# Kernel tuning notes

Hardware: AMD Instinct MI355X
Metric: run time of the kernel (lower is better)

Reference implementation:

```python
import jax, jax.numpy as jnp
import numpy as np

EPS = 1e-5
CIN = [3, 24, 48, 96, 192]
COUT = [24, 48, 96, 192, 384]
P = 512
NUM_CLASSES = 101
FC_IN = 384 * 16 * 3 * 3  # 55296


def _poly_layer(x, proj, alpha, gamma, beta):
    # x: (B, C, D, H, W)
    B, C, D, H, W = x.shape
    # im2col: 3x3x3 patches with zero padding 1 -> (B, C*27, D, H, W)
    patches = jax.lax.conv_general_dilated_patches(
        x, filter_shape=(3, 3, 3), window_strides=(1, 1, 1),
        padding=[(1, 1), (1, 1), (1, 1)])
    patches = jnp.moveaxis(patches, 1, -1)  # (B, D, H, W, C*27)
    ws = jnp.einsum('bdhwk,pk->bdhwp', patches, proj)      # projector GEMM
    out = jnp.einsum('bdhwp,po->bdhwo', ws, alpha)         # alpha GEMM
    out = jnp.maximum(1.0 + out, 0.0)                      # clamp(1+x, min=0)
    out = jnp.moveaxis(out, -1, 1)                         # (B, O, D, H, W)
    # MaxPool3d kernel/stride (1,2,2)
    out = jax.lax.reduce_window(out, -jnp.inf, jax.lax.max,
                                (1, 1, 1, 2, 2), (1, 1, 1, 2, 2), 'VALID')
    # BatchNorm3d with batch statistics (train-mode math)
    mean = out.mean(axis=(0, 2, 3, 4), keepdims=True)
    var = out.var(axis=(0, 2, 3, 4), keepdims=True)
    out = (out - mean) * jax.lax.rsqrt(var + EPS)
    out = out * gamma.reshape(1, -1, 1, 1, 1) + beta.reshape(1, -1, 1, 1, 1)
    return out


def setup_inputs() -> dict:
    key = jax.random.key(0)
    keys = jax.random.split(key, 32)
    inp = {'x': jax.random.normal(keys[0], (2, 3, 16, 112, 112), dtype=jnp.float32)}
    ki = 1
    for i in range(5):
        k_feat = CIN[i] * 27
        inp[f'p{i+1}'] = jax.random.normal(keys[ki], (P, k_feat), dtype=jnp.float32) / np.sqrt(k_feat); ki += 1
        inp[f'a{i+1}'] = jax.random.normal(keys[ki], (P, COUT[i]), dtype=jnp.float32) * np.sqrt(2.0 / COUT[i]); ki += 1
        inp[f'g{i+1}'] = jnp.ones((COUT[i],), dtype=jnp.float32)
        inp[f'q{i+1}'] = jnp.zeros((COUT[i],), dtype=jnp.float32)
    inp['w1'] = jax.random.normal(keys[ki], (512, FC_IN), dtype=jnp.float32) * np.sqrt(2.0 / 512); ki += 1
    inp['b1'] = jnp.zeros((512,), dtype=jnp.float32)
    inp['w2'] = jax.random.normal(keys[ki], (256, 512), dtype=jnp.float32) * np.sqrt(2.0 / 256); ki += 1
    inp['b2'] = jnp.zeros((256,), dtype=jnp.float32)
    inp['w3'] = jax.random.normal(keys[ki], (NUM_CLASSES, 256), dtype=jnp.float32) * np.sqrt(2.0 / NUM_CLASSES); ki += 1
    inp['b3'] = jnp.zeros((NUM_CLASSES,), dtype=jnp.float32)
    return inp


def reference(x, p1, a1, g1, q1, p2, a2, g2, q2, p3, a3, g3, q3,
              p4, a4, g4, q4, p5, a5, g5, q5, w1, b1, w2, b2, w3, b3):
    projs = [p1, p2, p3, p4, p5]
    alphas = [a1, a2, a3, a4, a5]
    gammas = [g1, g2, g3, g4, g5]
    betas = [q1, q2, q3, q4, q5]
    h = x
    for i in range(5):
        h = _poly_layer(h, projs[i], alphas[i], gammas[i], betas[i])
    h = h.reshape(h.shape[0], -1)  # (B, 55296)
    h = jax.nn.relu(h @ w1.T + b1)  # dropout = identity (eval)
    h = jax.nn.relu(h @ w2.T + b2)
    logits = h @ w3.T + b3
    return logits
```

## Files before the change

kernel.cpp:

```cpp
#include <hip/hip_runtime.h>

#define EPS_BN 1e-5f

typedef __attribute__((ext_vector_type(8))) short sh8;
typedef __attribute__((ext_vector_type(4))) short sh4;
typedef __attribute__((ext_vector_type(4))) float f32x4;

static const size_t PART_OFF = 2645784;
static const size_t PRE_OFF  = 6258456;
static const size_t OUT5_OFF = 8666904;
static const size_t H_OFF    = 8777496;
static const size_t ST_OFF   = 8888088;
static const size_t BNP_OFF  = 8888856;
static const size_t H1_OFF   = 8938008;
static const size_t WS_TOT   = 8939032;
__device__ __align__(256) float g_ws[WS_TOT];

static const size_t XIN_OFF = 0;
static const size_t A1_OFF  = 1871424;
static const size_t A2_OFF  = 4776768;
static const size_t A3_OFF  = 6331968;
static const size_t A4_OFF  = 7216704;
static const size_t AR_TOT  = 7776576;
__device__ __align__(256) unsigned short g_act[AR_TOT];

static const size_t WB_OFF[5] = {0, 4096, 36352, 162304, 659968};
static const size_t WB_TOT    = 2650624;
__device__ __align__(256) unsigned short g_wb[WB_TOT];

__device__ inline unsigned short f2bf(float v) {
    unsigned u = __float_as_uint(v);
    return (unsigned short)((u + 0x7fffu + ((u >> 16) & 1u)) >> 16);
}
__device__ inline float bf2f(unsigned short h) {
    return __uint_as_float(((unsigned)h) << 16);
}

__global__ __launch_bounds__(256) void init_input(const float* __restrict__ x,
                                                  unsigned short* __restrict__ xp,
                                                  float* __restrict__ bnp,
                                                  int4* __restrict__ zp, int nz,
                                                  int4* __restrict__ wbz, int nwb)
{
    const int i = blockIdx.x * 256 + threadIdx.x;
    if (i < nz) zp[i] = make_int4(0, 0, 0, 0);
    if (i < nwb) wbz[i] = make_int4(0, 0, 0, 0);
    if (i < 49152) bnp[i] = 0.f;
    if (i >= 2 * 18 * 114 * 114 * 4) return;
    const int c = i & 3;
    int t = i >> 2;
    const int xx = t % 114; t /= 114;
    const int yy = t % 114; t /= 114;
    const int zz = t % 18;
    const int b  = t / 18;
    float v = 0.f;
    if (c < 3 && (unsigned)(zz - 1) < 16u && (unsigned)(yy - 1) < 112u && (unsigned)(xx - 1) < 112u)
        v = x[(((size_t)b * 3 + c) * 16 + (zz - 1)) * 12544 + (yy - 1) * 112 + (xx - 1)];
    xp[i] = f2bf(v);
}

struct PrepArgs {
    const float* src[10];
    int W[10];
    int dstrow[10];
    int start[11];
    int rowtot;
};

__global__ __launch_bounds__(256) void prep_t(PrepArgs a, unsigned short* __restrict__ dst)
{
    __shared__ unsigned short tileh[32 * 72];
    __shared__ unsigned short tilel[32 * 72];
    int m = 0;
    {
        const int bx = blockIdx.x;
        while (m < 9 && bx >= a.start[m + 1]) ++m;
    }
    const int t  = blockIdx.x - a.start[m];
    const int tw = t >> 4, tp = t & 15;
    const int p0 = tp * 32, w0 = tw * 64;
    const int W = a.W[m];
    const float* __restrict__ src = a.src[m];
    const int tid = threadIdx.x;

    #pragma unroll
    for (int e = 0; e < 8; ++e) {
        const int idx = tid + e * 256;
        const int w = idx & 63, pr = idx >> 6;
        const int gw = w0 + w;
        float v = 0.f;
        if (gw < W) v = src[(size_t)(p0 + pr) * W + gw];
        const unsigned short hh = f2bf(v);
        tileh[pr * 72 + w] = hh;
        tilel[pr * 72 + w] = f2bf(v - bf2f(hh));
    }
    __syncthreads();
    {
        const int wr = tid >> 2, pg = (tid & 3) * 8;
        sh8 packh, packl;
        #pragma unroll
        for (int e = 0; e < 8; ++e) {
            packh[e] = (short)tileh[(pg + e) * 72 + wr];
            packl[e] = (short)tilel[(pg + e) * 72 + wr];
        }
        const size_t rh = (size_t)a.dstrow[m] + w0 + wr;
        *(sh8*)&dst[rh * 512 + p0 + pg] = packh;
        *(sh8*)&dst[(rh + a.rowtot) * 512 + p0 + pg] = packl;
    }
}

struct Fuse3Args {
    int aoff[5], poff[5];
    int woff[5];
    int KL[5];
    int noft[5];
    int kt[5];
    int start[6];
    int rowtot;
};

__global__ __launch_bounds__(256) void fuse_mfma(const unsigned short* __restrict__ tb,
                                                 unsigned short* __restrict__ wlin,
                                                 Fuse3Args a)
{
    int l = 0;
    {
        const int bx = blockIdx.x;
        while (l < 4 && bx >= a.start[l + 1]) ++l;
    }
    const int idx = blockIdx.x - a.start[l];
    const int ot = idx / a.kt[l];
    const int kt = idx % a.kt[l];
    const int lane = threadIdx.x & 63;
    const int wv = threadIdx.x >> 6;
    const size_t LOFF = (size_t)a.rowtot * 512;
    const int f = ot * 4 + wv;
    if (f >= a.noft[l]) return;

    const unsigned short* arow = tb + ((size_t)(a.aoff[l] + f * 16 + (lane & 15))) * 512 + (lane >> 4) * 8;
    const unsigned short* brow = tb + ((size_t)(a.poff[l] + kt * 64 + (lane & 15))) * 512 + (lane >> 4) * 8;

    f32x4 acc[4];
    #pragma unroll
    for (int i = 0; i < 4; ++i) acc[i] = (f32x4){0.f, 0.f, 0.f, 0.f};

    #pragma unroll 2
    for (int p0 = 0; p0 < 512; p0 += 32) {
        const sh8 ah  = *(const sh8*)(arow + p0);
        const sh8 alo = *(const sh8*)(arow + LOFF + p0);
        #pragma unroll
        for (int nt = 0; nt < 4; ++nt) {
            const sh8 bh = *(const sh8*)(brow + (size_t)nt * 16 * 512 + p0);
            const sh8 bl = *(const sh8*)(brow + LOFF + (size_t)nt * 16 * 512 + p0);
            acc[nt] = __builtin_amdgcn_mfma_f32_16x16x32_bf16(ah, bh, acc[nt], 0, 0, 0);
            acc[nt] = __builtin_amdgcn_mfma_f32_16x16x32_bf16(ah, bl, acc[nt], 0, 0, 0);
            acc[nt] = __builtin_amdgcn_mfma_f32_16x16x32_bf16(alo, bh, acc[nt], 0, 0, 0);
        }
    }

    const int KL = a.KL[l];
    unsigned short* wrow = wlin + a.woff[l];
    #pragma unroll
    for (int nt = 0; nt < 4; ++nt) {
        const int k = kt * 64 + nt * 16 + (lane & 15);
        #pragma unroll
        for (int j = 0; j < 4; ++j) {
            const int o = f * 16 + (lane >> 4) * 4 + j;
            wrow[(size_t)o * KL + k] = f2bf(acc[nt][j]);
        }
    }
}

struct ReordBArgs {
    int woff[5], wboff[5];
    int K[5], KL[5], KP[5], CP[5];
    int start[6];
};

__global__ __launch_bounds__(256) void reorder_b(const unsigned short* __restrict__ wlin,
                                                 unsigned short* __restrict__ wb,
                                                 ReordBArgs a)
{
    __shared__ __align__(16) unsigned short lds[5184];
    int l = 0;
    {
        const int bx = blockIdx.x;
        while (l < 4 && bx >= a.start[l + 1]) ++l;
    }
    const int o = blockIdx.x - a.start[l];
    const int K = a.K[l], KL = a.KL[l], KP = a.KP[l], CP = a.CP[l];
    const int tid = threadIdx.x;
    for (int i = tid; i < KP; i += 256) lds[i] = 0;
    __syncthreads();
    const unsigned short* src = wlin + a.woff[l] + (size_t)o * KL;
    for (int k = tid; k < K; k += 256) {
        const int c = k / 27, s = k - c * 27;
        lds[s * CP + c] = src[k];
    }
    __syncthreads();
    unsigned short* drow = wb + a.wboff[l] + (size_t)o * KP;
    for (int i = tid * 8; i < KP; i += 2048)
        *(sh8*)&drow[i] = *(const sh8*)&lds[i];
}

template<int CPAD, int COUT, int KPAD, int HI, int WI, int HP, int WP, int NBLK, int SPLIT>
__global__ __launch_bounds__(256) void conv_mfma(
    const unsigned short* __restrict__ in, const unsigned short* __restrict__ Wb,
    float* __restrict__ outf, float* __restrict__ part, float* __restrict__ bnp)
{
    constexpr int NT = NBLK / 16;
    constexpr int HI2 = HI + 2, WI2 = WI + 2;
    constexpr bool C8 = (CPAD % 8 == 0);
    constexpr int TABN = C8 ? KPAD / 8 : KPAD / 4;
    constexpr int NSTEP = KPAD / 32 / SPLIT;
    constexpr int MTOT = 2 * 16 * HP * WP * 4;
    constexpr bool BONCE = (NBLK * KPAD * 2 <= 16384);
    constexpr int BROW = BONCE ? (KPAD + 8) : 40;
    constexpr int BS_ELEMS = BONCE ? NBLK * BROW : 2 * NBLK * 40;

    __shared__ __align__(16) unsigned short As[2][128 * 40];
    __shared__ __align__(16) unsigned short Bs[BS_ELEMS];
    __shared__ int tab[TABN];
    __shared__ float bs[(SPLIT == 1) ? 2 * NBLK : 1];

    const int tid = threadIdx.x;
    const int lane = tid & 63;
    const int wv = tid >> 6;
    const int blk_m = blockIdx.x;
    const int oc0 = blockIdx.y * NBLK;
    const int kc = (SPLIT > 1) ? blockIdx.z : 0;

    for (int i = tid; i < TABN; i += 256) {
        const int k = i * (C8 ? 8 : 4);
        const int s = k / CPAD, c = k % CPAD;
        tab[i] = (s < 27) ? ((((s / 9) * HI2 + (s % 9) / 3) * WI2 + (s % 3)) * CPAD + c) : -1;
    }

    if constexpr (BONCE) {
        for (int i = tid; i < NBLK * KPAD / 8; i += 256) {
            const int r = i / (KPAD / 8), kk = i - r * (KPAD / 8);
            *(sh8*)&Bs[r * BROW + kk * 8] = *(const sh8*)&Wb[(size_t)(oc0 + r) * KPAD + kk * 8];
        }
    }

    const int srow = tid >> 1;
    const int half = tid & 1;
    const int m_g = blk_m * 128 + srow;
    const int pooled_s = m_g >> 2, sub_s = m_g & 3;
    const int pw_g = pooled_s % WP;
    const int ph_g = (pooled_s / WP) % HP;
    const int d_g  = (pooled_s / (WP * HP)) & 15;
    const int b_g  = pooled_s / (WP * HP * 16);
    const int h_g = 2 * ph_g + (sub_s >> 1);
    const int w_g = 2 * pw_g + (sub_s & 1);
    const size_t base_m = ((((size_t)b_g * 18 + d_g) * HI2 + h_g) * WI2 + w_g) * CPAD;

    const int brow = tid >> 2, bcc = tid & 3;
    const bool bload = (tid < NBLK * 4);

    f32x4 acc[2][NT];
    #pragma unroll
    for (int mf = 0; mf < 2; ++mf)
        #pragma unroll
        for (int i = 0; i < NT; ++i) acc[mf][i] = (f32x4){0.f, 0.f, 0.f, 0.f};

    const int k_begin = kc * NSTEP * 32;

    sh8 aA0, aA1;
    sh4 aP0, aP1, aP2, aP3;
    sh8 brg;

    __syncthreads();

    {
        const int k0 = k_begin;
        if constexpr (C8) {
            const int o0 = tab[(k0 >> 3) + half * 2];
            const int o1 = tab[(k0 >> 3) + half * 2 + 1];
            aA0 = (sh8){0, 0, 0, 0, 0, 0, 0, 0};
            aA1 = (sh8){0, 0, 0, 0, 0, 0, 0, 0};
            if (o0 >= 0) aA0 = *(const sh8*)(in + base_m + o0);
            if (o1 >= 0) aA1 = *(const sh8*)(in + base_m + o1);
            *(sh8*)&As[0][srow * 40 + (half * 2) * 8]     = aA0;
            *(sh8*)&As[0][srow * 40 + (half * 2 + 1) * 8] = aA1;
        } else {
            const int t0 = tab[(k0 >> 2) + half * 4];
            const int t1 = tab[(k0 >> 2) + half * 4 + 1];
            const int t2 = tab[(k0 >> 2) + half * 4 + 2];
            const int t3 = tab[(k0 >> 2) + half * 4 + 3];
            aP0 = (sh4){0, 0, 0, 0}; aP1 = (sh4){0, 0, 0, 0};
            aP2 = (sh4){0, 0, 0, 0}; aP3 = (sh4){0, 0, 0, 0};
            if (t0 >= 0) aP0 = *(const sh4*)(in + base_m + t0);
            if (t1 >= 0) aP1 = *(const sh4*)(in + base_m + t1);
            if (t2 >= 0) aP2 = *(const sh4*)(in + base_m + t2);
            if (t3 >= 0) aP3 = *(const sh4*)(in + base_m + t3);
            *(sh4*)&As[0][srow * 40 + (half * 4) * 4]     = aP0;
            *(sh4*)&As[0][srow * 40 + (half * 4 + 1) * 4] = aP1;
            *(sh4*)&As[0][srow * 40 + (half * 4 + 2) * 4] = aP2;
            *(sh4*)&As[0][srow * 40 + (half * 4 + 3) * 4] = aP3;
        }
        if constexpr (!BONCE) {
            if (bload) {
                brg = *(const sh8*)&Wb[(size_t)(oc0 + brow) * KPAD + k0 + bcc * 8];
                *(sh8*)&Bs[0 + brow * 40 + bcc * 8] = brg;
            }
        }
    }
    __syncthreads();

    int cur = 0;
    for (int s = 0; s < NSTEP; ++s) {
        const int k0 = k_begin + s * 32;
        if (s + 1 < NSTEP) {
            const int kn = k0 + 32;
            if constexpr (C8) {
                const int o0 = tab[(kn >> 3) + half * 2];
                const int o1 = tab[(kn >> 3) + half * 2 + 1];
                aA0 = (sh8){0, 0, 0, 0, 0, 0, 0, 0};
                aA1 = (sh8){0, 0, 0, 0, 0, 0, 0, 0};
                if (o0 >= 0) aA0 = *(const sh8*)(in + base_m + o0);
                if (o1 >= 0) aA1 = *(const sh8*)(in + base_m + o1);
            } else {
                const int t0 = tab[(kn >> 2) + half * 4];
                const int t1 = tab[(kn >> 2) + half * 4 + 1];
                const int t2 = tab[(kn >> 2) + half * 4 + 2];
                const int t3 = tab[(kn >> 2) + half * 4 + 3];
                aP0 = (sh4){0, 0, 0, 0}; aP1 = (sh4){0, 0, 0, 0};
                aP2 = (sh4){0, 0, 0, 0}; aP3 = (sh4){0, 0, 0, 0};
                if (t0 >= 0) aP0 = *(const sh4*)(in + base_m + t0);
                if (t1 >= 0) aP1 = *(const sh4*)(in + base_m + t1);
                if (t2 >= 0) aP2 = *(const sh4*)(in + base_m + t2);
                if (t3 >= 0) aP3 = *(const sh4*)(in + base_m + t3);
            }
            if constexpr (!BONCE) {
                if (bload) brg = *(const sh8*)&Wb[(size_t)(oc0 + brow) * KPAD + kn + bcc * 8];
            }
        }
        const sh8 af0 = *(const sh8*)&As[cur][(wv * 16 + (lane & 15)) * 40 + (lane >> 4) * 8];
        const sh8 af1 = *(const sh8*)&As[cur][(64 + wv * 16 + (lane & 15)) * 40 + (lane >> 4) * 8];
        #pragma unroll
        for (int nt = 0; nt < NT; ++nt) {
            sh8 bf;
            if constexpr (BONCE)
                bf = *(const sh8*)&Bs[(nt * 16 + (lane & 15)) * BROW + k0 + (lane >> 4) * 8];
            else
                bf = *(const sh8*)&Bs[cur * NBLK * 40 + (nt * 16 + (lane & 15)) * 40 + (lane >> 4) * 8];
            acc[0][nt] = __builtin_amdgcn_mfma_f32_16x16x32_bf16(af0, bf, acc[0][nt], 0, 0, 0);
            acc[1][nt] = __builtin_amdgcn_mfma_f32_16x16x32_bf16(af1, bf, acc[1][nt], 0, 0, 0);
        }
        if (s + 1 < NSTEP) {
            if constexpr (C8) {
                *(sh8*)&As[cur ^ 1][srow * 40 + (half * 2) * 8]     = aA0;
                *(sh8*)&As[cur ^ 1][srow * 40 + (half * 2 + 1) * 8] = aA1;
            } else {
                *(sh4*)&As[cur ^ 1][srow * 40 + (half * 4) * 4]     = aP0;
                *(sh4*)&As[cur ^ 1][srow * 40 + (half * 4 + 1) * 4] = aP1;
                *(sh4*)&As[cur ^ 1][srow * 40 + (half * 4 + 2) * 4] = aP2;
                *(sh4*)&As[cur ^ 1][srow * 40 + (half * 4 + 3) * 4] = aP3;
            }
            if constexpr (!BONCE) {
                if (bload) *(sh8*)&Bs[(cur ^ 1) * NBLK * 40 + brow * 40 + bcc * 8] = brg;
            }
        }
        __syncthreads();
        cur ^= 1;
    }

    const int q = lane >> 4;
    const int nloc = lane & 15;
    if constexpr (SPLIT == 1) {
        for (int i = tid; i < 2 * NBLK; i += 256) bs[i] = 0.f;
        __syncthreads();
        #pragma unroll
        for (int mf = 0; mf < 2; ++mf) {
            const int pooled_o = blk_m * 32 + mf * 16 + wv * 4 + q;
            #pragma unroll
            for (int nt = 0; nt < NT; ++nt) {
                const int oc = oc0 + nt * 16 + nloc;
                float mx = fmaxf(1.f + acc[mf][nt][0], 0.f);
                mx = fmaxf(mx, fmaxf(1.f + acc[mf][nt][1], 0.f));
                mx = fmaxf(mx, fmaxf(1.f + acc[mf][nt][2], 0.f));
                mx = fmaxf(mx, fmaxf(1.f + acc[mf][nt][3], 0.f));
                float s1 = 0.f;
                if (oc < COUT) {
                    outf[(size_t)pooled_o * COUT + oc] = mx;
                    s1 = mx;
                }
                float s2 = s1 * s1;
                s1 += __shfl_xor(s1, 16);
                s1 += __shfl_xor(s1, 32);
                s2 += __shfl_xor(s2, 16);
                s2 += __shfl_xor(s2, 32);
                if (q == 0) {
                    atomicAdd(&bs[nt * 16 + nloc], s1);
                    atomicAdd(&bs[NBLK + nt * 16 + nloc], s2);
                }
            }
        }
        __syncthreads();
        float* rowp = bnp + (size_t)(blk_m & 63) * 768;
        for (int i = tid; i < NBLK; i += 256) {
            const int oc = oc0 + i;
            if (oc < COUT) {
                atomicAdd(&rowp[oc], bs[i]);
                atomicAdd(&rowp[384 + oc], bs[NBLK + i]);
            }
        }
    } else {
        #pragma unroll
        for (int mf = 0; mf < 2; ++mf) {
            #pragma unroll
            for (int nt = 0; nt < NT; ++nt) {
                const int oc = oc0 + nt * 16 + nloc;
                #pragma unroll
                for (int r = 0; r < 4; ++r) {
                    const int mm = blk_m * 128 + mf * 64 + wv * 16 + q * 4 + r;
                    part[((size_t)kc * MTOT + mm) * COUT + oc] = acc[mf][nt][r];
                }
            }
        }
    }
}

template<int COUT, int HP, int WP, int SPLIT>
__global__ __launch_bounds__(256) void pool_epi(const float* __restrict__ part,
                                                float* __restrict__ outf,
                                                float* __restrict__ bnp)
{
    constexpr int PO = 2 * 16 * HP * WP;
    constexpr int M = PO * 4;
    __shared__ float bs[2 * COUT];
    const int tid = threadIdx.x;
    for (int i = tid; i < 2 * COUT; i += 256) bs[i] = 0.f;
    __syncthreads();
    const int idx = blockIdx.x * 256 + tid;
    if (idx < PO * COUT) {
        const int oc = idx % COUT;
        const int p = idx / COUT;
        float v[4] = {0.f, 0.f, 0.f, 0.f};
        for (int s = 0; s < SPLIT; ++s)
            #pragma unroll
            for (int r = 0; r < 4; ++r)
                v[r] += part[((size_t)s * M + p * 4 + r) * COUT + oc];
        float mx = fmaxf(1.f + v[0], 0.f);
        mx = fmaxf(mx, fmaxf(1.f + v[1], 0.f));
        mx = fmaxf(mx, fmaxf(1.f + v[2], 0.f));
        mx = fmaxf(mx, fmaxf(1.f + v[3], 0.f));
        outf[(size_t)p * COUT + oc] = mx;
        atomicAdd(&bs[oc], mx);
        atomicAdd(&bs[COUT + oc], mx * mx);
    }
    __syncthreads();
    float* rowp = bnp + (size_t)(blockIdx.x & 63) * 768;
    for (int i = tid; i < COUT; i += 256) {
        atomicAdd(&rowp[i], bs[i]);
        atomicAdd(&rowp[384 + i], bs[COUT + i]);
    }
}

__global__ __launch_bounds__(64) void bn_reduce(float* __restrict__ bnp,
                                                const float* __restrict__ gamma,
                                                const float* __restrict__ beta,
                                                float* __restrict__ st,
                                                float inv_n)
{
    const int c = blockIdx.x, tid = threadIdx.x;
    float s = bnp[(size_t)tid * 768 + c];
    float q = bnp[(size_t)tid * 768 + 384 + c];
    bnp[(size_t)tid * 768 + c] = 0.f;
    bnp[(size_t)tid * 768 + 384 + c] = 0.f;
    #pragma unroll
    for (int off = 32; off > 0; off >>= 1) {
        s += __shfl_down(s, off);
        q += __shfl_down(q, off);
    }
    if (tid == 0) {
        const float mean = s * inv_n;
        const float var  = q * inv_n - mean * mean;
        const float sc   = gamma[c] * rsqrtf(var + EPS_BN);
        st[2 * c]     = sc;
        st[2 * c + 1] = fmaf(-mean, sc, beta[c]);
    }
}

template<int C, int HP, int WP>
__global__ __launch_bounds__(256) void bn_apply_halo(const float* __restrict__ pre,
                                                     const float* __restrict__ st,
                                                     unsigned short* __restrict__ outh)
{
    constexpr int PO = 2 * 16 * HP * WP;
    const int idx = blockIdx.x * 256 + threadIdx.x;
    if (idx >= PO * C) return;
    const int c = idx % C;
    const int p = idx / C;
    const int pw = p % WP;
    const int ph = (p / WP) % HP;
    const int d  = (p / (WP * HP)) & 15;
    const int b  = p / (WP * HP * 16);
    const float v = fmaf(pre[idx], st[2 * c], st[2 * c + 1]);
    outh[((((size_t)b * 18 + d + 1) * (HP + 2) + ph + 1) * (WP + 2) + pw + 1) * C + c] = f2bf(v);
}

__global__ __launch_bounds__(256) void transpose5(const float* __restrict__ out5,
                                                  const float* __restrict__ st,
                                                  float* __restrict__ h)
{
    const int idx = blockIdx.x * 256 + threadIdx.x;
    if (idx >= 110592) return;
    const int c = idx % 384;
    const int p = idx / 384;
    const int b = p / 144;
    const int sp = p % 144;
    h[(size_t)b * 55296 + c * 144 + sp] = fmaf(out5[idx], st[2 * c], st[2 * c + 1]);
}

__global__ __launch_bounds__(256) void fc1_k(const float* __restrict__ h,
                                             const float* __restrict__ w1,
                                             const float* __restrict__ b1,
                                             float* __restrict__ hout)
{
    __shared__ float r0[256];
    __shared__ float r1[256];
    const int j = blockIdx.x, tid = threadIdx.x;
    const float* wr = w1 + (size_t)j * 55296;
    float a0 = 0.f, a1 = 0.f;
    for (int k = tid * 4; k < 55296; k += 1024) {
        const float4 w = *(const float4*)(wr + k);
        const float4 u = *(const float4*)(h + k);
        const float4 v = *(const float4*)(h + 55296 + k);
        a0 += w.x * u.x + w.y * u.y + w.z * u.z + w.w * u.w;
        a1 += w.x * v.x + w.y * v.y + w.z * v.z + w.w * v.w;
    }
    r0[tid] = a0; r1[tid] = a1;
    __syncthreads();
    for (int off = 128; off > 0; off >>= 1) {
        if (tid < off) { r0[tid] += r0[tid + off]; r1[tid] += r1[tid + off]; }
        __syncthreads();
    }
    if (tid == 0) {
        hout[j]       = fmaxf(r0[0] + b1[j], 0.f);
        hout[512 + j] = fmaxf(r1[0] + b1[j], 0.f);
    }
}

__global__ __launch_bounds__(256) void fc23_k(const float* __restrict__ h1,
                                              const float* __restrict__ w2,
                                              const float* __restrict__ b2,
                                              const float* __restrict__ w3,
                                              const float* __restrict__ b3,
                                              float* __restrict__ out)
{
    __shared__ float h1s[1024];
    __shared__ float h2[512];
    const int tid = threadIdx.x;
    for (int i = tid; i < 1024; i += 256) h1s[i] = h1[i];
    __syncthreads();
    {
        const float* wr = w2 + (size_t)tid * 512;
        #pragma unroll
        for (int b = 0; b < 2; ++b) {
            float a = 0.f;
            const float* hh = h1s + b * 512;
            for (int k = 0; k < 512; ++k) a = fmaf(wr[k], hh[k], a);
            h2[b * 256 + tid] = fmaxf(a + b2[tid], 0.f);
        }
    }
    __syncthreads();
    if (tid < 101) {
        const float* wr = w3 + (size_t)tid * 256;
        #pragma unroll
        for (int b = 0; b < 2; ++b) {
            float a = 0.f;
            const float* hh = h2 + b * 256;
            for (int k = 0; k < 256; ++k) a = fmaf(wr[k], hh[k], a);
            out[b * 101 + tid] = a + b3[tid];
        }
    }
}

extern "C" void kernel_launch(void* const* d_in, const int* in_sizes, int n_in,
                              void* d_out, int out_size, void* d_ws, size_t ws_size,
                              hipStream_t stream)
{
    const float* x  = (const float*)d_in[0];
    const float* p[5], *al[5], *g[5], *q[5];
    for (int i = 0; i < 5; ++i) {
        p[i]  = (const float*)d_in[1 + 4 * i];
        al[i] = (const float*)d_in[2 + 4 * i];
        g[i]  = (const float*)d_in[3 + 4 * i];
        q[i]  = (const float*)d_in[4 + 4 * i];
    }
    const float* w1 = (const float*)d_in[21];
    const float* b1 = (const float*)d_in[22];
    const float* w2 = (const float*)d_in[23];
    const float* b2 = (const float*)d_in[24];
    const float* w3 = (const float*)d_in[25];
    const float* b3 = (const float*)d_in[26];

    float* ws = nullptr;
    hipGetSymbolAddress((void**)&ws, HIP_SYMBOL(g_ws));
    unsigned short* act = nullptr;
    hipGetSymbolAddress((void**)&act, HIP_SYMBOL(g_act));
    unsigned short* wb = nullptr;
    hipGetSymbolAddress((void**)&wb, HIP_SYMBOL(g_wb));

    float* part = ws + PART_OFF;
    float* pre  = ws + PRE_OFF;
    float* out5 = ws + OUT5_OFF;
    float* h    = ws + H_OFF;
    float* st   = ws + ST_OFF;
    float* bnp  = ws + BNP_OFF;
    float* h1   = ws + H1_OFF;
    unsigned short* tbuf = (unsigned short*)ws;
    unsigned short* wlin = tbuf + (size_t)2 * 10816 * 512;

    unsigned short* xin = act + XIN_OFF;
    unsigned short* a1  = act + A1_OFF;
    unsigned short* a2  = act + A2_OFF;
    unsigned short* a3  = act + A3_OFF;
    unsigned short* a4  = act + A4_OFF;

    static const int KF[5] = {81, 648, 1296, 2592, 5184};
    static const int CO[5] = {24, 48, 96, 192, 384};
    static const int CP[5] = {4, 24, 48, 96, 192};
    static const int KP[5] = {128, 672, 1312, 2592, 5184};
    static const int APAD[5] = {64, 64, 128, 192, 384};
    static const int PPAD[5] = {128, 704, 1344, 2624, 5184};
    static const int KT[5] = {2, 11, 21, 41, 81};
    static const int OT[5] = {1, 1, 2, 3, 6};
    static const int NOFT[5] = {2, 3, 6, 12, 24};
    static const int NPAD[5] = {32, 48, 96, 192, 384};

    {
        const int nz = (int)((AR_TOT - A1_OFF) * 2 / 16);
        const int nwb = (int)(WB_TOT * 2 / 16);
        init_input<<<(2 * 18 * 114 * 114 * 4 + 255) / 256, 256, 0, stream>>>(
            x, xin, bnp, (int4*)(act + A1_OFF), nz, (int4*)wb, nwb);
    }

    PrepArgs pa;
    Fuse3Args f3;
    ReordBArgs rb;
    {
        int row = 0, blk = 0;
        pa.start[0] = 0;
        for (int i = 0; i < 5; ++i) {
            pa.src[i] = al[i]; pa.W[i] = CO[i]; pa.dstrow[i] = row;
            f3.aoff[i] = row;
            row += APAD[i];
            blk += (APAD[i] / 64) * 16;
            pa.start[i + 1] = blk;
        }
        for (int i = 0; i < 5; ++i) {
            pa.src[5 + i] = p[i]; pa.W[5 + i] = KF[i]; pa.dstrow[5 + i] = row;
            f3.poff[i] = row;
            row += PPAD[i];
            blk += (PPAD[i] / 64) * 16;
            pa.start[5 + i + 1] = blk;
        }
        pa.rowtot = row;
        f3.rowtot = row;
        prep_t<<<blk, 256, 0, stream>>>(pa, tbuf);
    }

    {
        int s0 = 0, woff = 0;
        for (int i = 0; i < 5; ++i) {
            f3.woff[i] = woff;
            f3.KL[i] = KT[i] * 64;
            f3.noft[i] = NOFT[i];
            f3.kt[i] = KT[i];
            f3.start[i] = s0;
            s0 += OT[i] * KT[i];
            woff += NPAD[i] * KT[i] * 64;
        }
        f3.start[5] = s0;
        fuse_mfma<<<s0, 256, 0, stream>>>(tbuf, wlin, f3);
    }

    {
        int s0 = 0, woff = 0;
        for (int i = 0; i < 5; ++i) {
            rb.woff[i] = woff;
            rb.wboff[i] = (int)WB_OFF[i];
            rb.K[i] = KF[i]; rb.KL[i] = KT[i] * 64; rb.KP[i] = KP[i]; rb.CP[i] = CP[i];
            rb.start[i] = s0;
            s0 += CO[i];
            woff += NPAD[i] * KT[i] * 64;
        }
        rb.start[5] = s0;
        reorder_b<<<s0, 256, 0, stream>>>(wlin, wb, rb);
    }

    conv_mfma<4, 24, 128, 112, 112, 56, 56, 32, 1>
        <<<dim3(3136, 1), 256, 0, stream>>>(xin, wb + WB_OFF[0], pre, nullptr, bnp);
    bn_reduce<<<24, 64, 0, stream>>>(bnp, g[0], q[0], st, 1.f / 100352.f);
    bn_apply_halo<24, 56, 56><<<9408, 256, 0, stream>>>(pre, st, a1);

    conv_mfma<24, 48, 672, 56, 56, 28, 28, 48, 1>
        <<<dim3(784, 1), 256, 0, stream>>>(a1, wb + WB_OFF[1], pre, nullptr, bnp);
    bn_reduce<<<48, 64, 0, stream>>>(bnp, g[1], q[1], st, 1.f / 25088.f);
    bn_apply_halo<48, 28, 28><<<4704, 256, 0, stream>>>(pre, st, a2);

    conv_mfma<48, 96, 1312, 28, 28, 14, 14, 48, 1>
        <<<dim3(196, 2), 256, 0, stream>>>(a2, wb + WB_OFF[2], pre, nullptr, bnp);
    bn_reduce<<<96, 64, 0, stream>>>(bnp, g[2], q[2], st, 1.f / 6272.f);
    bn_apply_halo<96, 14, 14><<<2352, 256, 0, stream>>>(pre, st, a3);

    conv_mfma<96, 192, 2592, 14, 14, 7, 7, 64, 3>
        <<<dim3(49, 3, 3), 256, 0, stream>>>(a3, wb + WB_OFF[3], nullptr, part, bnp);
    pool_epi<192, 7, 7, 3><<<1176, 256, 0, stream>>>(part, pre, bnp);
    bn_reduce<<<192, 64, 0, stream>>>(bnp, g[3], q[3], st, 1.f / 1568.f);
    bn_apply_halo<192, 7, 7><<<1176, 256, 0, stream>>>(pre, st, a4);

    conv_mfma<192, 384, 5184, 7, 7, 3, 3, 64, 6>
        <<<dim3(9, 6, 6), 256, 0, stream>>>(a4, wb + WB_OFF[4], nullptr, part, bnp);
    pool_epi<384, 3, 3, 6><<<432, 256, 0, stream>>>(part, out5, bnp);
    bn_reduce<<<384, 64, 0, stream>>>(bnp, g[4], q[4], st, 1.f / 288.f);

    transpose5<<<(110592 + 255) / 256, 256, 0, stream>>>(out5, st, h);
    fc1_k<<<512, 256, 0, stream>>>(h, w1, b1, h1);
    fc23_k<<<1, 256, 0, stream>>>(h1, w2, b2, w3, b3, (float*)d_out);
}
```

Baseline: 530.6 us.

## Stage fuse_mfma operand tiles through double-buffered LDS

The fuse_mfma kernel, which multiplies the alpha and projector matrices in split-bf16 form, now cooperatively loads 64x32 tiles of A and B (high and low parts) into padded, double-buffered shared memory. Previously each wave read its B tiles straight from global memory, so the four waves fetched the same data redundantly. Register prefetch of the next slice overlaps global loads with the MFMAs. The cost is a barrier per k-step and about 40KB of LDS per block. Waves beyond noft still take part in loading and only skip the store.

```diff
diff --git a/kernel.cpp b/kernel.cpp
--- a/kernel.cpp
+++ b/kernel.cpp
@@ -123,6 +123,11 @@
                                                  unsigned short* __restrict__ wlin,
                                                  Fuse3Args a)
 {
+    __shared__ __align__(16) unsigned short Ah[2][64 * 40];
+    __shared__ __align__(16) unsigned short Al[2][64 * 40];
+    __shared__ __align__(16) unsigned short Bh[2][64 * 40];
+    __shared__ __align__(16) unsigned short Bl[2][64 * 40];
+
     int l = 0;
     {
         const int bx = blockIdx.x;
@@ -131,42 +136,75 @@
     const int idx = blockIdx.x - a.start[l];
     const int ot = idx / a.kt[l];
     const int kt = idx % a.kt[l];
-    const int lane = threadIdx.x & 63;
-    const int wv = threadIdx.x >> 6;
+    const int tid = threadIdx.x;
+    const int lane = tid & 63;
+    const int wv = tid >> 6;
     const size_t LOFF = (size_t)a.rowtot * 512;
-    const int f = ot * 4 + wv;
-    if (f >= a.noft[l]) return;
-
-    const unsigned short* arow = tb + ((size_t)(a.aoff[l] + f * 16 + (lane & 15))) * 512 + (lane >> 4) * 8;
-    const unsigned short* brow = tb + ((size_t)(a.poff[l] + kt * 64 + (lane & 15))) * 512 + (lane >> 4) * 8;
+
+    const int srow = tid >> 2, spg = (tid & 3) * 8;
+    const unsigned short* asrc = tb + ((size_t)(a.aoff[l] + ot * 64 + srow)) * 512 + spg;
+    const unsigned short* bsrc = tb + ((size_t)(a.poff[l] + kt * 64 + srow)) * 512 + spg;
+    const int sidx = srow * 40 + spg;
 
     f32x4 acc[4];
     #pragma unroll
     for (int i = 0; i < 4; ++i) acc[i] = (f32x4){0.f, 0.f, 0.f, 0.f};
 
-    #pragma unroll 2
-    for (int p0 = 0; p0 < 512; p0 += 32) {
-        const sh8 ah  = *(const sh8*)(arow + p0);
-        const sh8 alo = *(const sh8*)(arow + LOFF + p0);
+    sh8 rah, ral, rbh, rbl;
+
+    rah = *(const sh8*)(asrc);
+    ral = *(const sh8*)(asrc + LOFF);
+    rbh = *(const sh8*)(bsrc);
+    rbl = *(const sh8*)(bsrc + LOFF);
+    *(sh8*)&Ah[0][sidx] = rah;
+    *(sh8*)&Al[0][sidx] = ral;
+    *(sh8*)&Bh[0][sidx] = rbh;
+    *(sh8*)&Bl[0][sidx] = rbl;
+    __syncthreads();
+
+    const int fr = (wv * 16 + (lane & 15)) * 40 + (lane >> 4) * 8;
+    int cur = 0;
+    for (int s = 0; s < 16; ++s) {
+        if (s + 1 < 16) {
+            const int pn = (s + 1) * 32;
+            rah = *(const sh8*)(asrc + pn);
+            ral = *(const sh8*)(asrc + LOFF + pn);
+            rbh = *(const sh8*)(bsrc + pn);
+            rbl = *(const sh8*)(bsrc + LOFF + pn);
+        }
+        const sh8 ah  = *(const sh8*)&Ah[cur][fr];
+        const sh8 alo = *(const sh8*)&Al[cur][fr];
         #pragma unroll
         for (int nt = 0; nt < 4; ++nt) {
-            const sh8 bh = *(const sh8*)(brow + (size_t)nt * 16 * 512 + p0);
-            const sh8 bl = *(const sh8*)(brow + LOFF + (size_t)nt * 16 * 512 + p0);
+            const int bidx = (nt * 16 + (lane & 15)) * 40 + (lane >> 4) * 8;
+            const sh8 bh = *(const sh8*)&Bh[cur][bidx];
+            const sh8 bl = *(const sh8*)&Bl[cur][bidx];
             acc[nt] = __builtin_amdgcn_mfma_f32_16x16x32_bf16(ah, bh, acc[nt], 0, 0, 0);
             acc[nt] = __builtin_amdgcn_mfma_f32_16x16x32_bf16(ah, bl, acc[nt], 0, 0, 0);
             acc[nt] = __builtin_amdgcn_mfma_f32_16x16x32_bf16(alo, bh, acc[nt], 0, 0, 0);
         }
-    }
-
-    const int KL = a.KL[l];
-    unsigned short* wrow = wlin + a.woff[l];
-    #pragma unroll
-    for (int nt = 0; nt < 4; ++nt) {
-        const int k = kt * 64 + nt * 16 + (lane & 15);
-        #pragma unroll
-        for (int j = 0; j < 4; ++j) {
-            const int o = f * 16 + (lane >> 4) * 4 + j;
-            wrow[(size_t)o * KL + k] = f2bf(acc[nt][j]);
+        if (s + 1 < 16) {
+            *(sh8*)&Ah[cur ^ 1][sidx] = rah;
+            *(sh8*)&Al[cur ^ 1][sidx] = ral;
+            *(sh8*)&Bh[cur ^ 1][sidx] = rbh;
+            *(sh8*)&Bl[cur ^ 1][sidx] = rbl;
+        }
+        __syncthreads();
+        cur ^= 1;
+    }
+
+    const int f = ot * 4 + wv;
+    if (f < a.noft[l]) {
+        const int KL = a.KL[l];
+        unsigned short* wrow = wlin + a.woff[l];
+        #pragma unroll
+        for (int nt = 0; nt < 4; ++nt) {
+            const int k = kt * 64 + nt * 16 + (lane & 15);
+            #pragma unroll
+            for (int j = 0; j < 4; ++j) {
+                const int o = f * 16 + (lane >> 4) * 4 + j;
+                wrow[(size_t)o * KL + k] = f2bf(acc[nt][j]);
+            }
         }
     }
 }
```

Result: faster. 499.3 us (-5.9%).
